# Kernel optimization log

Measured on AMD Instinct MI355X. Metric: run time of the kernel, lower is better.

## Reference

```python
import jax, jax.numpy as jnp
import numpy as np

N_NODES = 10000
N_EDGES = 320000
MUL = 32            # multiplicity of each input/output irrep
RADIAL = 8          # edge scalar (radial basis) dim
HID = 64            # fc_neurons widths
NUM_NEIGHBORS = 32.0
MIX = np.pi / 8.0
INV_SQRT2 = 1.0 / np.sqrt(2.0)   # per-path alpha: 2 paths feed each mid irrep
INV_SQRT3 = 1.0 / np.sqrt(3.0)   # w3j(1,1,0) normalization


def setup_inputs() -> dict:
    key = jax.random.key(0)
    ks = jax.random.split(key, 16)
    inp = {
        "node_input": jax.random.normal(ks[0], (N_NODES, 4 * MUL), jnp.float32),  # 32x0e+32x1o flat
        "edge_attr": jax.random.normal(ks[1], (N_EDGES, 4), jnp.float32),          # 1x0e+1x1o (sh l=0,1)
        "edge_scalar_attr": jax.random.uniform(ks[2], (N_EDGES, RADIAL), jnp.float32),
        # first linear: 32x0e+32x1o -> (32x0e+32x1o) + (32x0e+32x1o); columns [:MUL]=conv path, [MUL:]=self path
        "W1_0e": jax.random.normal(ks[3], (MUL, 2 * MUL), jnp.float32),
        "W1_1o": jax.random.normal(ks[4], (MUL, 2 * MUL), jnp.float32),
        # radial MLP
        "W_mlp1": jax.random.normal(ks[5], (RADIAL, HID), jnp.float32),
        "W_mlp2": jax.random.normal(ks[6], (HID, HID), jnp.float32),
        # per-instruction 'uvu' path weights (mul_v = 1 squeezed): shape (HID, MUL)
        "Wp_00": jax.random.normal(ks[7], (HID, MUL), jnp.float32),  # 0e x 0e -> 0e
        "Wp_01": jax.random.normal(ks[8], (HID, MUL), jnp.float32),  # 0e x 1o -> 1o
        "Wp_10": jax.random.normal(ks[9], (HID, MUL), jnp.float32),  # 1o x 0e -> 1o
        "Wp_11": jax.random.normal(ks[10], (HID, MUL), jnp.float32), # 1o x 1o -> 0e
        # final linear: 64x0e+64x1o -> 32x0e+32x1o
        "W2_0e": jax.random.normal(ks[11], (2 * MUL, MUL), jnp.float32),
        "W2_1o": jax.random.normal(ks[12], (2 * MUL, MUL), jnp.float32),
        "edge_src": jax.random.randint(ks[13], (N_EDGES,), 0, N_NODES, jnp.int32),
        "edge_dst": jax.random.randint(ks[14], (N_EDGES,), 0, N_NODES, jnp.int32),
    }
    return inp


def _forward(node_input, edge_attr, edge_scalar_attr,
             W1_0e, W1_1o, W_mlp1, W_mlp2,
             Wp_00, Wp_01, Wp_10, Wp_11, W2_0e, W2_1o,
             edge_src, edge_dst):
    N = node_input.shape[0]
    # split flat node features into irrep blocks: 32x0e (N,32), 32x1o (N,32,3)
    x0 = node_input[:, :MUL]
    x1 = node_input[:, MUL:].reshape(N, MUL, 3)

    # ---- equivariant Linear: input -> input + output (fan-in normalized) ----
    f0 = (x0 @ W1_0e) / np.sqrt(MUL)                           # (N, 2*MUL)
    f1 = jnp.einsum('nui,uw->nwi', x1, W1_1o) / np.sqrt(MUL)   # (N, 2*MUL, 3)
    feat0, self0 = f0[:, :MUL], f0[:, MUL:]
    feat1, self1 = f1[:, :MUL], f1[:, MUL:]

    # ---- gather to edges ----
    e0 = feat0[edge_src]        # (E, MUL)
    e1 = feat1[edge_src]        # (E, MUL, 3)
    ea0 = edge_attr[:, :1]      # (E, 1) 0e
    ea1 = edge_attr[:, 1:4]     # (E, 3) 1o

    # ---- radial MLP -> per-edge per-path weights ----
    h = jax.nn.gelu((edge_scalar_attr @ W_mlp1) / np.sqrt(RADIAL))
    h = jax.nn.gelu((h @ W_mlp2) / np.sqrt(HID))               # (E, HID)
    w00 = h @ Wp_00   # (E, MUL)
    w01 = h @ Wp_01
    w10 = h @ Wp_10
    w11 = h @ Wp_11

    # ---- CG tensor product, 'uvu' mode (mul_v = 1) ----
    out0_a = w00 * e0 * ea0                                   # 0e x 0e -> 0e   (E, MUL)
    out0_b = w11 * jnp.sum(e1 * ea1[:, None, :], -1) * INV_SQRT3  # 1o.1o -> 0e
    out1_a = (w01 * e0)[:, :, None] * ea1[:, None, :]         # 0e x 1o -> 1o   (E, MUL, 3)
    out1_b = (w10[:, :, None] * e1) * ea0[:, :, None]         # 1o x 0e -> 1o
    mid0 = jnp.concatenate([out0_a, out0_b], axis=1) * INV_SQRT2  # (E, 2*MUL)   64x0e
    mid1 = jnp.concatenate([out1_a, out1_b], axis=1) * INV_SQRT2  # (E, 2*MUL, 3) 64x1o

    # ---- scatter-add to destination nodes ----
    n0 = jax.ops.segment_sum(mid0, edge_dst, num_segments=N) / np.sqrt(NUM_NEIGHBORS)
    n1 = jax.ops.segment_sum(mid1, edge_dst, num_segments=N) / np.sqrt(NUM_NEIGHBORS)

    # ---- final equivariant Linear: 64x0e+64x1o -> 32x0e+32x1o ----
    conv0 = (n0 @ W2_0e) / np.sqrt(2 * MUL)                    # (N, MUL)
    conv1 = jnp.einsum('nui,uw->nwi', n1, W2_1o) / np.sqrt(2 * MUL)  # (N, MUL, 3)

    c, s = np.cos(MIX), np.sin(MIX)
    y0 = c * self0 + s * conv0
    y1 = c * self1 + s * conv1
    return jnp.concatenate([y0, y1.reshape(N, MUL * 3)], axis=1)  # (N, 128)


def reference(node_input, edge_attr, edge_scalar_attr,
              W1_0e, W1_1o, W_mlp1, W_mlp2,
              Wp_00, Wp_01, Wp_10, Wp_11, W2_0e, W2_1o,
              edge_src, edge_dst):
    return _forward(node_input, edge_attr, edge_scalar_attr,
                    W1_0e, W1_1o, W_mlp1, W_mlp2,
                    Wp_00, Wp_01, Wp_10, Wp_11, W2_0e, W2_1o,
                    edge_src, edge_dst)
```

## Files before the change

kernel.cpp:

```cpp
#include <hip/hip_runtime.h>

typedef unsigned int uint32;
typedef unsigned short ushrt;
typedef __attribute__((ext_vector_type(4))) float f32x4;
typedef __attribute__((ext_vector_type(2))) float f32x2;
typedef __attribute__((ext_vector_type(8))) _Float16 halfx8;
typedef __attribute__((ext_vector_type(4))) uint32 uint32x4;

#define N_NODES 10000
#define N_EDGES 320000

#define SC_W1      0.17677669529663687f
#define SC_MLP1    0.35355339059327373f
#define SC_MLP2    0.125f
#define INV_SQRT3  0.5773502691896258f
#define COS_MIX    0.9238795325112867f
#define SIN_CONV   0.04783542904563623f

#define WS_FEATP 0
#define I_CNT    1280000
#define I_OFF    1290016
#define U_REC    1300032
#define U_WF     2580032
#define U_WBUF   2587200

__device__ __forceinline__ uint32 packh2(float a, float b) {
    _Float16 ha = (_Float16)a, hb = (_Float16)b;
    return (uint32)__builtin_bit_cast(unsigned short, ha) |
           ((uint32)__builtin_bit_cast(unsigned short, hb) << 16);
}
__device__ __forceinline__ unsigned short h16(float x) {
    _Float16 h = (_Float16)x;
    return __builtin_bit_cast(unsigned short, h);
}
__device__ __forceinline__ unsigned short pack_fp8_2(float a, float b) {
    return (unsigned short)(__builtin_amdgcn_cvt_pk_fp8_f32(a, b, 0, false) & 0xffff);
}
__device__ __forceinline__ float gelu_fast(float x) {
    float x2 = x * x;
    float z = x * __builtin_fmaf(0.03567740814f, x2, 0.7978845608f);
    float E = __builtin_amdgcn_exp2f(z * -2.885390082f);
    return x * __builtin_amdgcn_rcpf(1.0f + E);
}

#define K1_CNT_BLOCKS  1250
#define K1_PREP_BLOCKS 7
__global__ __launch_bounds__(256) void k1_fused(
        const int* __restrict__ edge_dst, int* __restrict__ cnt,
        const float* __restrict__ Wm1, const float* __restrict__ Wm2,
        const float* __restrict__ Wp00, const float* __restrict__ Wp01,
        const float* __restrict__ Wp10, const float* __restrict__ Wp11,
        uint32* __restrict__ wf) {
    int b = blockIdx.x;
    if (b < K1_CNT_BLOCKS) {
        int e = b * 256 + threadIdx.x;
        atomicAdd(&cnt[edge_dst[e]], 1);
    } else {
        int gid = (b - K1_CNT_BLOCKS) * 256 + threadIdx.x;
        int f = gid >> 6, lane = gid & 63;
        int kq = (lane >> 4) * 8;
        int c15 = lane & 15;
        float vals[8];
        if (f < 4) {
            int c = 16 * f + c15;
#pragma unroll
            for (int j = 0; j < 8; ++j) { int k = kq + j; vals[j] = (k < 8) ? Wm1[k * 64 + c] : 0.f; }
        } else if (f < 12) {
            int idx = f - 4, nt = idx >> 1, ks = idx & 1;
            int c = 16 * nt + c15;
#pragma unroll
            for (int j = 0; j < 8; ++j) { int k = 32 * ks + kq + j; vals[j] = Wm2[k * 64 + c]; }
        } else {
            int idx = f - 12, nt = idx >> 1, ks = idx & 1;
            int c = 16 * nt + c15;
            int u = c & 31, m = c >> 5;
            const float* W = (m == 0) ? Wp00 : (m == 1) ? Wp01 : (m == 2) ? Wp10 : Wp11;
            float sc = (m == 3) ? 0.125f * INV_SQRT3 : 0.125f;
#pragma unroll
            for (int j = 0; j < 8; ++j) { int k = 32 * ks + kq + j; vals[j] = W[k * 32 + u] * sc; }
        }
        uint32* o = wf + f * 256 + lane * 4;
#pragma unroll
        for (int w = 0; w < 4; ++w) o[w] = packh2(vals[2 * w], vals[2 * w + 1]);
    }
}

__global__ __launch_bounds__(1024) void csr_scan(const int* __restrict__ cnt,
                                                 int* __restrict__ off) {
    __shared__ int partial[1024];
    int t = threadIdx.x;
    const int CHUNK = 10;
    int base = t * CHUNK;
    int s = 0;
#pragma unroll
    for (int j = 0; j < CHUNK; ++j) {
        int idx = base + j;
        s += (idx < N_NODES) ? cnt[idx] : 0;
    }
    partial[t] = s;
    __syncthreads();
    for (int o = 1; o < 1024; o <<= 1) {
        int v = partial[t];
        int add = (t >= o) ? partial[t - o] : 0;
        __syncthreads();
        partial[t] = v + add;
        __syncthreads();
    }
    int run = (t > 0) ? partial[t - 1] : 0;
    for (int j = 0; j < CHUNK; ++j) {
        int idx = base + j;
        if (idx < N_NODES) {
            off[idx] = run;
            run += cnt[idx];
        }
    }
    if (t == 1023) off[N_NODES] = run;
}

#define MLP_BLOCKS 1250
#define K3_NODE_BLOCKS 2500
__global__ __launch_bounds__(256, 3) void k3_fused(
        const float* __restrict__ edge_scalar, const float* __restrict__ edge_attr,
        const int* __restrict__ src_in, const int* __restrict__ dst_in,
        int* __restrict__ off,
        const uint32* __restrict__ wf,
        uint32* __restrict__ wbuf, uint4* __restrict__ rec,
        const float* __restrict__ x,
        const float* __restrict__ W1_0e, const float* __restrict__ W1_1o,
        float* __restrict__ featp, float* __restrict__ out) {
    __shared__ uint32x4 wfl[28 * 64];
    __shared__ unsigned short sh[4][1024];
    __shared__ float eaxs[4][16];
    __shared__ int   poss[4][16];
    __shared__ float xrow[4][128];

    int lane = threadIdx.x & 63;
    int wvq = threadIdx.x >> 6;

    if (blockIdx.x >= MLP_BLOCKS) {
        int node = (blockIdx.x - MLP_BLOCKS) * 4 + wvq;
        float2 v = *(const float2*)(x + (size_t)node * 128 + lane * 2);
        xrow[wvq][lane * 2]     = v.x;
        xrow[wvq][lane * 2 + 1] = v.y;
        __syncthreads();
        const float* sx = xrow[wvq];
        int w = lane;
        float f0 = 0.f, f1x = 0.f, f1y = 0.f, f1z = 0.f;
#pragma unroll
        for (int u = 0; u < 32; ++u) {
            float w0 = W1_0e[u * 64 + w];
            float w1 = W1_1o[u * 64 + w];
            f0  += sx[u] * w0;
            f1x += sx[32 + u * 3 + 0] * w1;
            f1y += sx[32 + u * 3 + 1] * w1;
            f1z += sx[32 + u * 3 + 2] * w1;
        }
        f0 *= SC_W1; f1x *= SC_W1; f1y *= SC_W1; f1z *= SC_W1;
        if (w < 32) {
            featp[node * 128 + w]      = f0;
            featp[node * 128 + 32 + w] = f1x;
            featp[node * 128 + 64 + w] = f1y;
            featp[node * 128 + 96 + w] = f1z;
        } else {
            int ww = w - 32;
            out[node * 128 + ww] = COS_MIX * f0;
            out[node * 128 + 32 + ww * 3 + 0] = COS_MIX * f1x;
            out[node * 128 + 32 + ww * 3 + 1] = COS_MIX * f1y;
            out[node * 128 + 32 + ww * 3 + 2] = COS_MIX * f1z;
        }
        return;
    }

    {
        const uint32x4* s = (const uint32x4*)wf;
        for (int i = threadIdx.x; i < 28 * 64; i += 256) wfl[i] = s[i];
    }
    __syncthreads();

    int wave_id = blockIdx.x * 4 + wvq;
    int kq = (lane >> 4) * 8;
    int r15 = lane & 15;

    const f32x4 z4 = {0.f, 0.f, 0.f, 0.f};
    unsigned short* shw = sh[wvq];
    uint32* obw = (uint32*)shw;
    unsigned short* obw16 = (unsigned short*)obw;

    for (int g = wave_id; g < N_EDGES / 16; g += MLP_BLOCKS * 4) {
        int e0 = g * 16;

        halfx8 a0 = (halfx8)0;
        if (lane < 16) {
            int e = e0 + lane;
            const float* esp = edge_scalar + (size_t)e * 8;
            float4 p = *(const float4*)esp;
            float4 q = *(const float4*)(esp + 4);
            float4 av = *(const float4*)(edge_attr + (size_t)e * 4);
            int dn = dst_in[e];
            int sn = src_in[e];
            int pos = atomicAdd(&off[dn], 1);
            poss[wvq][lane] = pos;
            eaxs[wvq][lane] = av.x;
            uint4 rv;
            rv.x = __float_as_uint(av.y);
            rv.y = __float_as_uint(av.z);
            rv.z = __float_as_uint(av.w);
            rv.w = (uint32)sn;
            rec[pos] = rv;
            a0[0] = (_Float16)p.x; a0[1] = (_Float16)p.y;
            a0[2] = (_Float16)p.z; a0[3] = (_Float16)p.w;
            a0[4] = (_Float16)q.x; a0[5] = (_Float16)q.y;
            a0[6] = (_Float16)q.z; a0[7] = (_Float16)q.w;
        }

        f32x4 acc1[4];
#pragma unroll
        for (int nt = 0; nt < 4; ++nt) {
            halfx8 bb = __builtin_bit_cast(halfx8, wfl[nt * 64 + lane]);
            acc1[nt] = __builtin_amdgcn_mfma_f32_16x16x32_f16(a0, bb, z4, 0, 0, 0);
        }
#pragma unroll
        for (int nt = 0; nt < 4; ++nt)
#pragma unroll
            for (int i = 0; i < 4; ++i) {
                float gv = gelu_fast(acc1[nt][i] * SC_MLP1);
                int rr = (lane >> 4) * 4 + i;
                int ix = rr * 64 + 16 * nt + r15;
                shw[ix ^ ((rr & 7) << 3)] = h16(gv);
            }
        halfx8 a1[2];
#pragma unroll
        for (int ks = 0; ks < 2; ++ks) {
            int ix = r15 * 64 + 32 * ks + kq;
            a1[ks] = __builtin_bit_cast(halfx8,
                       *(const uint32x4*)&shw[ix ^ ((r15 & 7) << 3)]);
        }

        f32x4 acc2[4];
#pragma unroll
        for (int nt = 0; nt < 4; ++nt) {
            halfx8 b0 = __builtin_bit_cast(halfx8, wfl[(4 + nt * 2 + 0) * 64 + lane]);
            halfx8 b1 = __builtin_bit_cast(halfx8, wfl[(4 + nt * 2 + 1) * 64 + lane]);
            acc2[nt] = __builtin_amdgcn_mfma_f32_16x16x32_f16(a1[0], b0, z4, 0, 0, 0);
            acc2[nt] = __builtin_amdgcn_mfma_f32_16x16x32_f16(a1[1], b1, acc2[nt], 0, 0, 0);
        }
#pragma unroll
        for (int nt = 0; nt < 4; ++nt)
#pragma unroll
            for (int i = 0; i < 4; ++i) {
                float gv = gelu_fast(acc2[nt][i] * SC_MLP2);
                int rr = (lane >> 4) * 4 + i;
                int ix = rr * 64 + 16 * nt + r15;
                shw[ix ^ ((rr & 7) << 3)] = h16(gv);
            }
        halfx8 a2[2];
#pragma unroll
        for (int ks = 0; ks < 2; ++ks) {
            int ix = r15 * 64 + 32 * ks + kq;
            a2[ks] = __builtin_bit_cast(halfx8,
                       *(const uint32x4*)&shw[ix ^ ((r15 & 7) << 3)]);
        }

        f32x4 accp[8];
#pragma unroll
        for (int nt = 0; nt < 8; ++nt) {
            halfx8 b0 = __builtin_bit_cast(halfx8, wfl[(12 + nt * 2 + 0) * 64 + lane]);
            halfx8 b1 = __builtin_bit_cast(halfx8, wfl[(12 + nt * 2 + 1) * 64 + lane]);
            accp[nt] = __builtin_amdgcn_mfma_f32_16x16x32_f16(a2[0], b0, z4, 0, 0, 0);
            accp[nt] = __builtin_amdgcn_mfma_f32_16x16x32_f16(a2[1], b1, accp[nt], 0, 0, 0);
        }

#pragma unroll
        for (int i = 0; i < 4; ++i) {
            int rr = (lane >> 4) * 4 + i;
            float eax = eaxs[wvq][rr];
            unsigned short* orow = obw16 + rr * 64;
            orow[r15]      = pack_fp8_2(accp[0][i] * eax, accp[2][i]);
            orow[16 + r15] = pack_fp8_2(accp[1][i] * eax, accp[3][i]);
            orow[32 + r15] = pack_fp8_2(accp[4][i] * eax, accp[6][i]);
            orow[48 + r15] = pack_fp8_2(accp[5][i] * eax, accp[7][i]);
        }
#pragma unroll
        for (int pass = 0; pass < 2; ++pass) {
            int r = pass * 8 + (lane >> 3);
            int pos = poss[wvq][r];
            int c4 = (lane & 7) * 4;
            uint32x4 v = *(const uint32x4*)&obw[r * 32 + c4];
            *(uint32x4*)(wbuf + (size_t)pos * 32 + c4) = v;
        }
    }
}

__global__ __launch_bounds__(256) void gather(const int* __restrict__ off,
                                              const int* __restrict__ cnt,
                                              const uint4* __restrict__ rec,
                                              const uint32* __restrict__ wbuf,
                                              const float* __restrict__ featp,
                                              const float* __restrict__ W2_0e,
                                              const float* __restrict__ W2_1o,
                                              float* __restrict__ out) {
    int wv = threadIdx.x >> 6;
    int lane = threadIdx.x & 63;
    int node = blockIdx.x * 4 + wv;
    int u = lane & 31;
    int half = lane >> 5;

    int end = __builtin_amdgcn_readfirstlane(off[node]);
    int beg = end - __builtin_amdgcn_readfirstlane(cnt[node]);

    float a0acc = 0.f, a1x = 0.f, a1y = 0.f, a1z = 0.f;
    int offA = u + half * 32, offB = 64 + u, offC = 96 + u;
    const ushrt* wbuf16 = (const ushrt*)wbuf;
    int uslot = (half << 5) + u;

    for (int i0 = beg; i0 < end; i0 += 64) {
        int nn = end - i0;
        if (nn > 64) nn = 64;
        int idx = i0 + ((lane < nn) ? lane : 0);
        uint4 rv = rec[idx];
        int eyv = (int)rv.x, ezv = (int)rv.y, ewv = (int)rv.z, svv = (int)rv.w;
        for (int j0 = 0; j0 < nn; j0 += 4) {
            uint32 wl_[4];
            float fa_[4], fb_[4], fc_[4], ey_[4], ez_[4], ew_[4];
#pragma unroll
            for (int t = 0; t < 4; ++t) {
                int j = j0 + t;
                int jc = (j < nn) ? j : nn - 1;
                ey_[t] = __uint_as_float((uint32)__builtin_amdgcn_readlane(eyv, jc));
                ez_[t] = __uint_as_float((uint32)__builtin_amdgcn_readlane(ezv, jc));
                ew_[t] = __uint_as_float((uint32)__builtin_amdgcn_readlane(ewv, jc));
                int s  = __builtin_amdgcn_readlane(svv, jc);
                uint32 wl = (uint32)wbuf16[(size_t)(i0 + jc) * 64 + uslot];
                wl_[t] = (j < nn) ? wl : 0u;
                const float* fp = featp + (size_t)s * 128;
                fa_[t] = fp[offA];
                fb_[t] = fp[offB];
                fc_[t] = fp[offC];
            }
#pragma unroll
            for (int t = 0; t < 4; ++t) {
                f32x2 wab = __builtin_amdgcn_cvt_pk_f32_fp8((int)wl_[t], false);
                float wa = wab.x;
                float wb = wab.y;
                float va = half ? ey_[t] : 1.0f;
                float vb = half ? ez_[t] : 0.0f;
                float vc = half ? ew_[t] : 0.0f;
                float dot = fa_[t] * va + fb_[t] * vb + fc_[t] * vc;
                float w0s = half ? wb : wa;
                a0acc += w0s * dot;
                float m  = half ? wa : wb * fa_[t];
                float vx = half ? fa_[t] : ey_[t];
                float vy = half ? fb_[t] : ez_[t];
                float vz = half ? fc_[t] : ew_[t];
                a1x += m * vx; a1y += m * vy; a1z += m * vz;
            }
        }
    }

    __shared__ float red[4][256];
    float* r = red[wv];
    int c = (half << 5) + u;
    r[c] = a0acc;
    int b = 64 + c * 3;
    r[b] = a1x; r[b + 1] = a1y; r[b + 2] = a1z;
    __syncthreads();

    if (half == 0) {
        float acc = 0.f;
#pragma unroll 8
        for (int w = 0; w < 64; ++w) acc += r[w] * W2_0e[w * 32 + u];
        int o = node * 128 + u;
        out[o] = out[o] + SIN_CONV * acc;
    } else {
        float c0 = 0.f, c1 = 0.f, c2 = 0.f;
#pragma unroll 8
        for (int w = 0; w < 64; ++w) {
            float bw = W2_1o[w * 32 + u];
            c0 += r[64 + w * 3 + 0] * bw;
            c1 += r[64 + w * 3 + 1] * bw;
            c2 += r[64 + w * 3 + 2] * bw;
        }
        int o = node * 128 + 32 + u * 3;
        out[o + 0] = out[o + 0] + SIN_CONV * c0;
        out[o + 1] = out[o + 1] + SIN_CONV * c1;
        out[o + 2] = out[o + 2] + SIN_CONV * c2;
    }
}

extern "C" void kernel_launch(void* const* d_in, const int* in_sizes, int n_in,
                              void* d_out, int out_size, void* d_ws, size_t ws_size,
                              hipStream_t stream) {
    const float* node_input  = (const float*)d_in[0];
    const float* edge_attr   = (const float*)d_in[1];
    const float* edge_scalar = (const float*)d_in[2];
    const float* W1_0e       = (const float*)d_in[3];
    const float* W1_1o       = (const float*)d_in[4];
    const float* W_mlp1      = (const float*)d_in[5];
    const float* W_mlp2      = (const float*)d_in[6];
    const float* Wp00        = (const float*)d_in[7];
    const float* Wp01        = (const float*)d_in[8];
    const float* Wp10        = (const float*)d_in[9];
    const float* Wp11        = (const float*)d_in[10];
    const float* W2_0e       = (const float*)d_in[11];
    const float* W2_1o       = (const float*)d_in[12];
    const int*   edge_src    = (const int*)d_in[13];
    const int*   edge_dst    = (const int*)d_in[14];
    float* ws   = (float*)d_ws;
    int*   wsI  = (int*)d_ws;
    uint32* wsU = (uint32*)d_ws;
    uint4* recp = (uint4*)(wsU + U_REC);
    float* outp = (float*)d_out;

    hipMemsetAsync(wsI + I_CNT, 0, (N_NODES + 1) * sizeof(int), stream);

    k1_fused<<<K1_CNT_BLOCKS + K1_PREP_BLOCKS, 256, 0, stream>>>(
        edge_dst, wsI + I_CNT,
        W_mlp1, W_mlp2, Wp00, Wp01, Wp10, Wp11, wsU + U_WF);
    csr_scan<<<1, 1024, 0, stream>>>(wsI + I_CNT, wsI + I_OFF);
    k3_fused<<<MLP_BLOCKS + K3_NODE_BLOCKS, 256, 0, stream>>>(
        edge_scalar, edge_attr, edge_src, edge_dst, wsI + I_OFF,
        wsU + U_WF, wsU + U_WBUF, recp,
        node_input, W1_0e, W1_1o, ws + WS_FEATP, outp);
    gather<<<N_NODES / 4, 256, 0, stream>>>(wsI + I_OFF, wsI + I_CNT, recp,
                                            wsU + U_WBUF, ws + WS_FEATP,
                                            W2_0e, W2_1o, outp);
}
```

Before: 120.2 us.

## Switch edge MLP to 32x32x16 MFMA tiles processing 32 edges per wave

Replaces the 16x16x32 MFMA sequence in the edge radial MLP and path-weight projection with 32x32x16 MFMAs, so each wave handles 32 edges per iteration instead of 16. The weight fragments are repacked for the new operand layout (26 fragments instead of 28, since the first layer's padded K shrinks), and the shared staging buffers double. The aim is fewer MFMA issues and less per-edge loop overhead. In exchange it raises accumulator register pressure (16-float accumulators) and LDS use, which may lower occupancy.

After: 113.3 us. -5.8%, faster.

```diff
diff --git a/kernel.cpp b/kernel.cpp
--- a/kernel.cpp
+++ b/kernel.cpp
@@ -3,6 +3,7 @@
 typedef unsigned int uint32;
 typedef unsigned short ushrt;
 typedef __attribute__((ext_vector_type(4))) float f32x4;
+typedef __attribute__((ext_vector_type(16))) float f32x16;
 typedef __attribute__((ext_vector_type(2))) float f32x2;
 typedef __attribute__((ext_vector_type(8))) _Float16 halfx8;
 typedef __attribute__((ext_vector_type(4))) uint32 uint32x4;
@@ -57,27 +58,26 @@
         atomicAdd(&cnt[edge_dst[e]], 1);
     } else {
         int gid = (b - K1_CNT_BLOCKS) * 256 + threadIdx.x;
+        if (gid >= 26 * 64) return;
         int f = gid >> 6, lane = gid & 63;
-        int kq = (lane >> 4) * 8;
-        int c15 = lane & 15;
+        int kb = (lane >> 5) * 8;
+        int c31 = lane & 31;
         float vals[8];
-        if (f < 4) {
-            int c = 16 * f + c15;
-#pragma unroll
-            for (int j = 0; j < 8; ++j) { int k = kq + j; vals[j] = (k < 8) ? Wm1[k * 64 + c] : 0.f; }
-        } else if (f < 12) {
-            int idx = f - 4, nt = idx >> 1, ks = idx & 1;
-            int c = 16 * nt + c15;
-#pragma unroll
-            for (int j = 0; j < 8; ++j) { int k = 32 * ks + kq + j; vals[j] = Wm2[k * 64 + c]; }
+        if (f < 2) {
+            int c = 32 * f + c31;
+#pragma unroll
+            for (int j = 0; j < 8; ++j) { int k = kb + j; vals[j] = (k < 8) ? Wm1[k * 64 + c] : 0.f; }
+        } else if (f < 10) {
+            int idx = f - 2, nc = idx >> 2, ks = idx & 3;
+            int c = 32 * nc + c31;
+#pragma unroll
+            for (int j = 0; j < 8; ++j) { int k = 16 * ks + kb + j; vals[j] = Wm2[k * 64 + c]; }
         } else {
-            int idx = f - 12, nt = idx >> 1, ks = idx & 1;
-            int c = 16 * nt + c15;
-            int u = c & 31, m = c >> 5;
+            int idx = f - 10, m = idx >> 2, ks = idx & 3;
             const float* W = (m == 0) ? Wp00 : (m == 1) ? Wp01 : (m == 2) ? Wp10 : Wp11;
             float sc = (m == 3) ? 0.125f * INV_SQRT3 : 0.125f;
 #pragma unroll
-            for (int j = 0; j < 8; ++j) { int k = 32 * ks + kq + j; vals[j] = W[k * 32 + u] * sc; }
+            for (int j = 0; j < 8; ++j) { int k = 16 * ks + kb + j; vals[j] = W[k * 32 + c31] * sc; }
         }
         uint32* o = wf + f * 256 + lane * 4;
 #pragma unroll
@@ -128,10 +128,10 @@
         const float* __restrict__ x,
         const float* __restrict__ W1_0e, const float* __restrict__ W1_1o,
         float* __restrict__ featp, float* __restrict__ out) {
-    __shared__ uint32x4 wfl[28 * 64];
-    __shared__ unsigned short sh[4][1024];
-    __shared__ float eaxs[4][16];
-    __shared__ int   poss[4][16];
+    __shared__ uint32x4 wfl[26 * 64];
+    __shared__ unsigned short sh[4][2048];
+    __shared__ float eaxs[4][32];
+    __shared__ int   poss[4][32];
     __shared__ float xrow[4][128];
 
     int lane = threadIdx.x & 63;
@@ -173,24 +173,24 @@
 
     {
         const uint32x4* s = (const uint32x4*)wf;
-        for (int i = threadIdx.x; i < 28 * 64; i += 256) wfl[i] = s[i];
+        for (int i = threadIdx.x; i < 26 * 64; i += 256) wfl[i] = s[i];
     }
     __syncthreads();
 
     int wave_id = blockIdx.x * 4 + wvq;
-    int kq = (lane >> 4) * 8;
-    int r15 = lane & 15;
-
-    const f32x4 z4 = {0.f, 0.f, 0.f, 0.f};
+    int l31 = lane & 31;
+    int lhi = lane >> 5;
+
+    const f32x16 z16 = {0,0,0,0,0,0,0,0,0,0,0,0,0,0,0,0};
     unsigned short* shw = sh[wvq];
     uint32* obw = (uint32*)shw;
-    unsigned short* obw16 = (unsigned short*)obw;
-
-    for (int g = wave_id; g < N_EDGES / 16; g += MLP_BLOCKS * 4) {
-        int e0 = g * 16;
+    unsigned short* obw16 = shw;
+
+    for (int g = wave_id; g < N_EDGES / 32; g += MLP_BLOCKS * 4) {
+        int e0 = g * 32;
 
         halfx8 a0 = (halfx8)0;
-        if (lane < 16) {
+        if (lane < 32) {
             int e = e0 + lane;
             const float* esp = edge_scalar + (size_t)e * 8;
             float4 p = *(const float4*)esp;
@@ -213,75 +213,76 @@
             a0[6] = (_Float16)q.z; a0[7] = (_Float16)q.w;
         }
 
-        f32x4 acc1[4];
-#pragma unroll
-        for (int nt = 0; nt < 4; ++nt) {
-            halfx8 bb = __builtin_bit_cast(halfx8, wfl[nt * 64 + lane]);
-            acc1[nt] = __builtin_amdgcn_mfma_f32_16x16x32_f16(a0, bb, z4, 0, 0, 0);
-        }
-#pragma unroll
-        for (int nt = 0; nt < 4; ++nt)
-#pragma unroll
-            for (int i = 0; i < 4; ++i) {
-                float gv = gelu_fast(acc1[nt][i] * SC_MLP1);
-                int rr = (lane >> 4) * 4 + i;
-                int ix = rr * 64 + 16 * nt + r15;
-                shw[ix ^ ((rr & 7) << 3)] = h16(gv);
-            }
-        halfx8 a1[2];
-#pragma unroll
-        for (int ks = 0; ks < 2; ++ks) {
-            int ix = r15 * 64 + 32 * ks + kq;
+        f32x16 acc1[2];
+#pragma unroll
+        for (int nc = 0; nc < 2; ++nc) {
+            halfx8 bb = __builtin_bit_cast(halfx8, wfl[nc * 64 + lane]);
+            acc1[nc] = __builtin_amdgcn_mfma_f32_32x32x16_f16(a0, bb, z16, 0, 0, 0);
+        }
+#pragma unroll
+        for (int nc = 0; nc < 2; ++nc)
+#pragma unroll
+            for (int reg = 0; reg < 16; ++reg) {
+                float gv = gelu_fast(acc1[nc][reg] * SC_MLP1);
+                int r = (reg & 3) + 8 * (reg >> 2) + 4 * lhi;
+                int ix = r * 64 + 32 * nc + l31;
+                shw[ix ^ ((r & 7) << 3)] = h16(gv);
+            }
+        halfx8 a1[4];
+#pragma unroll
+        for (int ks = 0; ks < 4; ++ks) {
+            int ix = l31 * 64 + 16 * ks + lhi * 8;
             a1[ks] = __builtin_bit_cast(halfx8,
-                       *(const uint32x4*)&shw[ix ^ ((r15 & 7) << 3)]);
-        }
-
-        f32x4 acc2[4];
-#pragma unroll
-        for (int nt = 0; nt < 4; ++nt) {
-            halfx8 b0 = __builtin_bit_cast(halfx8, wfl[(4 + nt * 2 + 0) * 64 + lane]);
-            halfx8 b1 = __builtin_bit_cast(halfx8, wfl[(4 + nt * 2 + 1) * 64 + lane]);
-            acc2[nt] = __builtin_amdgcn_mfma_f32_16x16x32_f16(a1[0], b0, z4, 0, 0, 0);
-            acc2[nt] = __builtin_amdgcn_mfma_f32_16x16x32_f16(a1[1], b1, acc2[nt], 0, 0, 0);
-        }
-#pragma unroll
-        for (int nt = 0; nt < 4; ++nt)
-#pragma unroll
-            for (int i = 0; i < 4; ++i) {
-                float gv = gelu_fast(acc2[nt][i] * SC_MLP2);
-                int rr = (lane >> 4) * 4 + i;
-                int ix = rr * 64 + 16 * nt + r15;
-                shw[ix ^ ((rr & 7) << 3)] = h16(gv);
-            }
-        halfx8 a2[2];
-#pragma unroll
-        for (int ks = 0; ks < 2; ++ks) {
-            int ix = r15 * 64 + 32 * ks + kq;
+                       *(const uint32x4*)&shw[ix ^ ((lane & 7) << 3)]);
+        }
+
+        f32x16 acc2[2];
+#pragma unroll
+        for (int nc = 0; nc < 2; ++nc) {
+            acc2[nc] = z16;
+#pragma unroll
+            for (int ks = 0; ks < 4; ++ks) {
+                halfx8 bb = __builtin_bit_cast(halfx8, wfl[(2 + nc * 4 + ks) * 64 + lane]);
+                acc2[nc] = __builtin_amdgcn_mfma_f32_32x32x16_f16(a1[ks], bb, acc2[nc], 0, 0, 0);
+            }
+        }
+#pragma unroll
+        for (int nc = 0; nc < 2; ++nc)
+#pragma unroll
+            for (int reg = 0; reg < 16; ++reg) {
+                float gv = gelu_fast(acc2[nc][reg] * SC_MLP2);
+                int r = (reg & 3) + 8 * (reg >> 2) + 4 * lhi;
+                int ix = r * 64 + 32 * nc + l31;
+                shw[ix ^ ((r & 7) << 3)] = h16(gv);
+            }
+        halfx8 a2[4];
+#pragma unroll
+        for (int ks = 0; ks < 4; ++ks) {
+            int ix = l31 * 64 + 16 * ks + lhi * 8;
             a2[ks] = __builtin_bit_cast(halfx8,
-                       *(const uint32x4*)&shw[ix ^ ((r15 & 7) << 3)]);
-        }
-
-        f32x4 accp[8];
-#pragma unroll
-        for (int nt = 0; nt < 8; ++nt) {
-            halfx8 b0 = __builtin_bit_cast(halfx8, wfl[(12 + nt * 2 + 0) * 64 + lane]);
-            halfx8 b1 = __builtin_bit_cast(halfx8, wfl[(12 + nt * 2 + 1) * 64 + lane]);
-            accp[nt] = __builtin_amdgcn_mfma_f32_16x16x32_f16(a2[0], b0, z4, 0, 0, 0);
-            accp[nt] = __builtin_amdgcn_mfma_f32_16x16x32_f16(a2[1], b1, accp[nt], 0, 0, 0);
-        }
-
-#pragma unroll
-        for (int i = 0; i < 4; ++i) {
-            int rr = (lane >> 4) * 4 + i;
-            float eax = eaxs[wvq][rr];
-            unsigned short* orow = obw16 + rr * 64;
-            orow[r15]      = pack_fp8_2(accp[0][i] * eax, accp[2][i]);
-            orow[16 + r15] = pack_fp8_2(accp[1][i] * eax, accp[3][i]);
-            orow[32 + r15] = pack_fp8_2(accp[4][i] * eax, accp[6][i]);
-            orow[48 + r15] = pack_fp8_2(accp[5][i] * eax, accp[7][i]);
-        }
-#pragma unroll
-        for (int pass = 0; pass < 2; ++pass) {
+                       *(const uint32x4*)&shw[ix ^ ((lane & 7) << 3)]);
+        }
+
+        f32x16 accp[4];
+#pragma unroll
+        for (int m = 0; m < 4; ++m) {
+            accp[m] = z16;
+#pragma unroll
+            for (int ks = 0; ks < 4; ++ks) {
+                halfx8 bb = __builtin_bit_cast(halfx8, wfl[(10 + m * 4 + ks) * 64 + lane]);
+                accp[m] = __builtin_amdgcn_mfma_f32_32x32x16_f16(a2[ks], bb, accp[m], 0, 0, 0);
+            }
+        }
+
+#pragma unroll
+        for (int reg = 0; reg < 16; ++reg) {
+            int r = (reg & 3) + 8 * (reg >> 2) + 4 * lhi;
+            float eax = eaxs[wvq][r];
+            obw16[r * 64 + l31]      = pack_fp8_2(accp[0][reg] * eax, accp[1][reg]);
+            obw16[r * 64 + 32 + l31] = pack_fp8_2(accp[2][reg] * eax, accp[3][reg]);
+        }
+#pragma unroll
+        for (int pass = 0; pass < 4; ++pass) {
             int r = pass * 8 + (lane >> 3);
             int pos = poss[wvq][r];
             int c4 = (lane & 7) * 4;
```
